# Optimization experiments

Hardware: AMD Instinct MI355X
Metric: run time of the kernel (lower is better)

Reference implementation:

```python
import jax, jax.numpy as jnp
import numpy as np


def setup_inputs() -> dict:
    key = jax.random.key(0)
    k1, k2 = jax.random.split(key)
    B, N = 16, 131072
    x = jax.random.normal(k1, (B, N, 3), dtype=jnp.float32)
    farthest_init = jax.random.randint(k2, (B,), 0, N)  # torch.randint(0, N, (B,))
    return {"x": x, "farthest_init": farthest_init, "npoint": 4096}


def reference(x, farthest_init, npoint):
    """Farthest point sampling: returns sampled point indices [B, npoint].

    npoint corresponds to keypoint_num = int(max(density * volume)) in the
    original module; it is shape-determining so it is passed as a static int.
    """
    xyz = x[:, :, :3]                      # [B, N, 3]
    B, N, _ = xyz.shape
    INF = jnp.float32(1e10)                # matches torch's 1e10 init distance

    def step(carry, _):
        distance, farthest = carry         # [B, N], [B]
        # gather current centroid per batch: xyz[b, farthest[b], :]
        centroid = jnp.take_along_axis(xyz, farthest[:, None, None], axis=1)  # [B,1,3]
        dist = jnp.sum((xyz - centroid) ** 2, axis=-1)  # [B, N]
        distance = jnp.minimum(distance, dist)          # masked update dist<distance
        new_farthest = jnp.argmax(distance, axis=-1)    # [B]
        return (distance, new_farthest), farthest       # emit index chosen this step

    init = (jnp.full((B, N), INF, dtype=xyz.dtype), farthest_init)
    _, centroids = jax.lax.scan(step, init, None, length=npoint)  # [npoint, B]
    return centroids.T                                            # [B, npoint]
```

## Files before the change

kernel.cpp:

```cpp
#include <hip/hip_runtime.h>
#include <stdint.h>

#define NBATCH 16
#define NPTS   131072
#define NPOINT 4096
#define KWG    16
#define TPB    512
#define NWAVE  (TPB/64)
#define PPT    (NPTS/(KWG*TPB))
#define SEG    (NPTS/KWG)
#define SEGSH  13

typedef unsigned long long u64;
typedef unsigned int u32;

template<int CTRL>
__device__ __forceinline__ u32 dpp32(u32 x) {
    return (u32)__builtin_amdgcn_update_dpp(0, (int)x, CTRL, 0xf, 0xf, true);
}
__device__ __forceinline__ u32 umax_(u32 a, u32 b) { return a > b ? a : b; }

template<int CTRL>
__device__ __forceinline__ u64 dpp64max(u64 x) {
    u32 lo = dpp32<CTRL>((u32)x);
    u32 hi = dpp32<CTRL>((u32)(x >> 32));
    u64 o = ((u64)hi << 32) | lo;
    return o > x ? o : x;
}
__device__ __forceinline__ u32 wave_umax(u32 x) {
    x = umax_(x, dpp32<0xB1>(x));
    x = umax_(x, dpp32<0x4E>(x));
    x = umax_(x, dpp32<0x124>(x));
    x = umax_(x, dpp32<0x128>(x));
    x = umax_(x, (u32)__builtin_amdgcn_ds_swizzle((int)x, 0x401F));
    x = umax_(x, (u32)__shfl_xor((int)x, 32, 64));
    return x;
}
__device__ __forceinline__ u64 row16_umax64(u64 k) {
    k = dpp64max<0xB1>(k);
    k = dpp64max<0x4E>(k);
    k = dpp64max<0x124>(k);
    k = dpp64max<0x128>(k);
    return k;
}

__global__ __launch_bounds__(TPB, 2) void fps_kernel(
    const float* __restrict__ xyz, const int* __restrict__ finit,
    int* __restrict__ out, u64* __restrict__ ring)
{
    const int b    = blockIdx.x >> 4;
    const int w    = blockIdx.x & 15;
    const int tid  = threadIdx.x;
    const int lane = tid & 63;
    const int wv   = tid >> 6;

    const float* xb = xyz + (size_t)b * NPTS * 3;
    const int base = w * SEG;

    float px[PPT], py[PPT], pz[PPT], pd[PPT];
    u32 inv[PPT];
    #pragma unroll
    for (int j = 0; j < PPT; ++j) {
        int idx = base + j * TPB + tid;
        px[j] = xb[(size_t)idx * 3 + 0];
        py[j] = xb[(size_t)idx * 3 + 1];
        pz[j] = xb[(size_t)idx * 3 + 2];
        pd[j] = 1e10f;
        inv[j] = (u32)(NPTS - 1 - idx);
    }

    __shared__ u64   lds_keys[NWAVE];
    __shared__ float bc[3];

    const int f0 = finit[b];
    if (w == 0 && tid == 0) out[b * NPOINT] = f0;
    float cx = xb[(size_t)f0 * 3 + 0];
    float cy = xb[(size_t)f0 * 3 + 1];
    float cz = xb[(size_t)f0 * 3 + 2];

    u64* bp = ring + (size_t)b * 2 * KWG;

    for (int t = 1; t < NPOINT; ++t) {
        float m0 = -1.0f, m1 = -1.0f, m2 = -1.0f, m3 = -1.0f;
        #pragma unroll
        for (int j = 0; j < PPT; ++j) {
            float dx = __fsub_rn(px[j], cx);
            float dy = __fsub_rn(py[j], cy);
            float dz = __fsub_rn(pz[j], cz);
            float d  = __fmaf_rn(dz, dz, __fmaf_rn(dy, dy, __fmul_rn(dx, dx)));
            float nd = fminf(pd[j], d);
            pd[j] = nd;
            if ((j & 3) == 0)      m0 = fmaxf(m0, nd);
            else if ((j & 3) == 1) m1 = fmaxf(m1, nd);
            else if ((j & 3) == 2) m2 = fmaxf(m2, nd);
            else                   m3 = fmaxf(m3, nd);
        }
        float mx = fmaxf(fmaxf(m0, m1), fmaxf(m2, m3));
        u32 mxb = wave_umax(__float_as_uint(mx));
        u32 b0 = 0, b1 = 0, b2 = 0, b3 = 0;
        #pragma unroll
        for (int j = 0; j < PPT; ++j) {
            bool tie = (__float_as_uint(pd[j]) == mxb);
            if ((j & 3) == 0)      b0 = tie ? umax_(b0, inv[j]) : b0;
            else if ((j & 3) == 1) b1 = tie ? umax_(b1, inv[j]) : b1;
            else if ((j & 3) == 2) b2 = tie ? umax_(b2, inv[j]) : b2;
            else                   b3 = tie ? umax_(b3, inv[j]) : b3;
        }
        u32 bv = wave_umax(umax_(umax_(b0, b1), umax_(b2, b3)));
        if (lane == 0)
            lds_keys[wv] = ((u64)mxb << 17) | (u64)bv;
        __syncthreads();

        const int p = t & 1;
        if (wv == 0) {
            const u64 tt = (u64)(u32)t;
            const u64 tg = tt << 49;
            u64 kb = lds_keys[lane & (NWAVE - 1)];
            kb = row16_umax64(kb);
            u64* bpp = bp + (p << 4);
            if (lane == 0)
                __hip_atomic_store(&bpp[w], tg | kb, __ATOMIC_RELAXED,
                                   __HIP_MEMORY_SCOPE_AGENT);
            u64 g = tg | kb;
            if (lane < 16 && lane != w) {
                u64* sp = &bpp[lane];
                u64 ga = __hip_atomic_load(sp, __ATOMIC_RELAXED, __HIP_MEMORY_SCOPE_AGENT);
                for (;;) {
                    u64 gb = __hip_atomic_load(sp, __ATOMIC_RELAXED, __HIP_MEMORY_SCOPE_AGENT);
                    if ((ga >> 49) == tt) { g = ga; break; }
                    ga = __hip_atomic_load(sp, __ATOMIC_RELAXED, __HIP_MEMORY_SCOPE_AGENT);
                    if ((gb >> 49) == tt) { g = gb; break; }
                }
            }
            float sxl = 0.f, syl = 0.f, szl = 0.f;
            if (lane < 16) {
                int bi_l = (NPTS - 1) - (int)(g & 0x1FFFF);
                sxl = xb[(size_t)bi_l * 3 + 0];
                syl = xb[(size_t)bi_l * 3 + 1];
                szl = xb[(size_t)bi_l * 3 + 2];
            }
            u64 K = row16_umax64((lane < 16) ? g : 0);
            if (lane < 16) {
                int bi    = (NPTS - 1) - (int)(K & 0x1FFFF);
                int Pstar = bi >> SEGSH;
                float cxn = __shfl(sxl, Pstar, 64);
                float cyn = __shfl(syl, Pstar, 64);
                float czn = __shfl(szl, Pstar, 64);
                if (lane == 0) {
                    bc[0] = cxn; bc[1] = cyn; bc[2] = czn;
                    if (w == 0) out[b * NPOINT + t] = bi;
                }
            }
        }
        __syncthreads();
        cx = bc[0]; cy = bc[1]; cz = bc[2];
    }
}

extern "C" void kernel_launch(void* const* d_in, const int* in_sizes, int n_in,
                              void* d_out, int out_size, void* d_ws, size_t ws_size,
                              hipStream_t stream) {
    const float* xyz   = (const float*)d_in[0];
    const int*   finit = (const int*)d_in[1];
    int*         out   = (int*)d_out;
    u64*         ring  = (u64*)d_ws;

    void* args[] = { (void*)&xyz, (void*)&finit, (void*)&out, (void*)&ring };
    dim3 grid(NBATCH * KWG), block(TPB);
    if (hipLaunchCooperativeKernel((const void*)fps_kernel, grid, block, args, 0, stream)
        != hipSuccess) {
        fps_kernel<<<grid, block, 0, stream>>>(xyz, finit, out, ring);
    }
}
```

Measured before the change: 7.814 ms.

## Publish per-wave argmax keys globally and drop intra-block barrier before exchange

Each wave now writes its own tagged max key straight into a per-batch global ring of 128 slots, instead of first combining keys in LDS behind a __syncthreads. Wave 0 of every workgroup polls all 128 slots, two per lane, and prefetches the candidate centroid coordinates as soon as both of its slots arrive. It then finishes the reduction with a full-wave 64-bit max and picks the winning lane by segment and wave index. The centroid broadcast buffer is double-buffered by parity so that one barrier per step is enough. The aim is to cut one block barrier and the LDS round trip per step, at the cost of eight times more global polling traffic and a larger workspace ring.

```diff
diff --git a/kernel.cpp b/kernel.cpp
--- a/kernel.cpp
+++ b/kernel.cpp
@@ -20,13 +20,6 @@
 }
 __device__ __forceinline__ u32 umax_(u32 a, u32 b) { return a > b ? a : b; }
 
-template<int CTRL>
-__device__ __forceinline__ u64 dpp64max(u64 x) {
-    u32 lo = dpp32<CTRL>((u32)x);
-    u32 hi = dpp32<CTRL>((u32)(x >> 32));
-    u64 o = ((u64)hi << 32) | lo;
-    return o > x ? o : x;
-}
 __device__ __forceinline__ u32 wave_umax(u32 x) {
     x = umax_(x, dpp32<0xB1>(x));
     x = umax_(x, dpp32<0x4E>(x));
@@ -36,11 +29,32 @@
     x = umax_(x, (u32)__shfl_xor((int)x, 32, 64));
     return x;
 }
-__device__ __forceinline__ u64 row16_umax64(u64 k) {
+template<int CTRL>
+__device__ __forceinline__ u64 dpp64max(u64 x) {
+    u32 lo = dpp32<CTRL>((u32)x);
+    u32 hi = dpp32<CTRL>((u32)(x >> 32));
+    u64 o = ((u64)hi << 32) | lo;
+    return o > x ? o : x;
+}
+__device__ __forceinline__ u64 swz64max(u64 x) {
+    u32 lo = (u32)__builtin_amdgcn_ds_swizzle((int)(u32)x, 0x401F);
+    u32 hi = (u32)__builtin_amdgcn_ds_swizzle((int)(u32)(x >> 32), 0x401F);
+    u64 o = ((u64)hi << 32) | lo;
+    return o > x ? o : x;
+}
+__device__ __forceinline__ u64 sx32max(u64 x) {
+    u32 lo = (u32)__shfl_xor((int)(u32)x, 32, 64);
+    u32 hi = (u32)__shfl_xor((int)(u32)(x >> 32), 32, 64);
+    u64 o = ((u64)hi << 32) | lo;
+    return o > x ? o : x;
+}
+__device__ __forceinline__ u64 wave_umax64(u64 k) {
     k = dpp64max<0xB1>(k);
     k = dpp64max<0x4E>(k);
     k = dpp64max<0x124>(k);
     k = dpp64max<0x128>(k);
+    k = swz64max(k);
+    k = sx32max(k);
     return k;
 }
 
@@ -69,8 +83,7 @@
         inv[j] = (u32)(NPTS - 1 - idx);
     }
 
-    __shared__ u64   lds_keys[NWAVE];
-    __shared__ float bc[3];
+    __shared__ float bc[2][3];
 
     const int f0 = finit[b];
     if (w == 0 && tid == 0) out[b * NPOINT] = f0;
@@ -78,7 +91,7 @@
     float cy = xb[(size_t)f0 * 3 + 1];
     float cz = xb[(size_t)f0 * 3 + 2];
 
-    u64* bp = ring + (size_t)b * 2 * KWG;
+    u64* bring = ring + (size_t)b * 2 * 128;
 
     for (int t = 1; t < NPOINT; ++t) {
         float m0 = -1.0f, m1 = -1.0f, m2 = -1.0f, m3 = -1.0f;
@@ -107,53 +120,52 @@
             else                   b3 = tie ? umax_(b3, inv[j]) : b3;
         }
         u32 bv = wave_umax(umax_(umax_(b0, b1), umax_(b2, b3)));
+
+        const int p  = t & 1;
+        const u64 tt = (u64)(u32)t;
+        const u64 tg = tt << 49;
+        u64* bpp = bring + (p << 7);
         if (lane == 0)
-            lds_keys[wv] = ((u64)mxb << 17) | (u64)bv;
-        __syncthreads();
+            __hip_atomic_store(&bpp[(w << 3) | wv],
+                               tg | ((u64)mxb << 17) | (u64)bv,
+                               __ATOMIC_RELAXED, __HIP_MEMORY_SCOPE_AGENT);
 
-        const int p = t & 1;
         if (wv == 0) {
-            const u64 tt = (u64)(u32)t;
-            const u64 tg = tt << 49;
-            u64 kb = lds_keys[lane & (NWAVE - 1)];
-            kb = row16_umax64(kb);
-            u64* bpp = bp + (p << 4);
-            if (lane == 0)
-                __hip_atomic_store(&bpp[w], tg | kb, __ATOMIC_RELAXED,
-                                   __HIP_MEMORY_SCOPE_AGENT);
-            u64 g = tg | kb;
-            if (lane < 16 && lane != w) {
-                u64* sp = &bpp[lane];
-                u64 ga = __hip_atomic_load(sp, __ATOMIC_RELAXED, __HIP_MEMORY_SCOPE_AGENT);
-                for (;;) {
-                    u64 gb = __hip_atomic_load(sp, __ATOMIC_RELAXED, __HIP_MEMORY_SCOPE_AGENT);
-                    if ((ga >> 49) == tt) { g = ga; break; }
-                    ga = __hip_atomic_load(sp, __ATOMIC_RELAXED, __HIP_MEMORY_SCOPE_AGENT);
-                    if ((gb >> 49) == tt) { g = gb; break; }
+            u64* sp0 = bpp + lane;
+            u64* sp1 = bpp + 64 + lane;
+            u64 ga = 0, gb = 0;
+            bool da = false, db = false, pf = false;
+            float sxl = 0.f, syl = 0.f, szl = 0.f;
+            for (;;) {
+                u64 va = da ? ga : __hip_atomic_load(sp0, __ATOMIC_RELAXED, __HIP_MEMORY_SCOPE_AGENT);
+                u64 vb = db ? gb : __hip_atomic_load(sp1, __ATOMIC_RELAXED, __HIP_MEMORY_SCOPE_AGENT);
+                if (!da && (va >> 49) == tt) { ga = va; da = true; }
+                if (!db && (vb >> 49) == tt) { gb = vb; db = true; }
+                if (da && db && !pf) {
+                    pf = true;
+                    u64 gm = ga > gb ? ga : gb;
+                    int bl = (NPTS - 1) - (int)(gm & 0x1FFFF);
+                    const float* cp = &xb[(size_t)bl * 3];
+                    sxl = cp[0]; syl = cp[1]; szl = cp[2];
+                    asm volatile("" : "+v"(sxl), "+v"(syl), "+v"(szl));
                 }
+                if (__all(da && db)) break;
             }
-            float sxl = 0.f, syl = 0.f, szl = 0.f;
-            if (lane < 16) {
-                int bi_l = (NPTS - 1) - (int)(g & 0x1FFFF);
-                sxl = xb[(size_t)bi_l * 3 + 0];
-                syl = xb[(size_t)bi_l * 3 + 1];
-                szl = xb[(size_t)bi_l * 3 + 2];
-            }
-            u64 K = row16_umax64((lane < 16) ? g : 0);
-            if (lane < 16) {
-                int bi    = (NPTS - 1) - (int)(K & 0x1FFFF);
-                int Pstar = bi >> SEGSH;
-                float cxn = __shfl(sxl, Pstar, 64);
-                float cyn = __shfl(syl, Pstar, 64);
-                float czn = __shfl(szl, Pstar, 64);
-                if (lane == 0) {
-                    bc[0] = cxn; bc[1] = cyn; bc[2] = czn;
-                    if (w == 0) out[b * NPOINT + t] = bi;
-                }
+            u64 g = ga > gb ? ga : gb;
+            u64 K  = wave_umax64(g);
+            int bi = (NPTS - 1) - (int)(K & 0x1FFFF);
+            int s     = ((bi >> SEGSH) << 3) | ((bi >> 6) & (NWAVE - 1));
+            int lstar = s & 63;
+            float cxn = __shfl(sxl, lstar, 64);
+            float cyn = __shfl(syl, lstar, 64);
+            float czn = __shfl(szl, lstar, 64);
+            if (lane == 0) {
+                bc[p][0] = cxn; bc[p][1] = cyn; bc[p][2] = czn;
+                if (w == 0) out[b * NPOINT + t] = bi;
             }
         }
         __syncthreads();
-        cx = bc[0]; cy = bc[1]; cz = bc[2];
+        cx = bc[p][0]; cy = bc[p][1]; cz = bc[p][2];
     }
 }
 
```

New measurement: 11.78 ms. 50.8% more time.

## Replace block barriers with tagged LDS flags and pass winner coordinates in keys

Applied to the files above, without the earlier changes.

Each wave now picks the coordinates of its own argmax candidate from registers and shuffles them out. It publishes the key and the coordinates as tagged 64-bit words in LDS. Wave 0 polls these words instead of waiting at `__syncthreads`, then exchanges key and coordinates with the peer workgroups through the global ring. This removes the dependent global gather of the winning point's xyz on every iteration. The other waves spin on a release/acquire-tagged broadcast slot instead of a second barrier, which takes both block-wide barriers off the serial critical path. The cost is more cross-workgroup ring traffic (four words per workgroup) and extra selection and shuffle work per step.

```diff
diff --git a/kernel.cpp b/kernel.cpp
--- a/kernel.cpp
+++ b/kernel.cpp
@@ -14,19 +14,18 @@
 typedef unsigned long long u64;
 typedef unsigned int u32;
 
+#define LDA(p)    __hip_atomic_load((p),  __ATOMIC_RELAXED, __HIP_MEMORY_SCOPE_AGENT)
+#define STA(p,v)  __hip_atomic_store((p),(v),__ATOMIC_RELAXED,__HIP_MEMORY_SCOPE_AGENT)
+#define LDW(p)    __hip_atomic_load((p),  __ATOMIC_RELAXED, __HIP_MEMORY_SCOPE_WORKGROUP)
+#define LDWA(p)   __hip_atomic_load((p),  __ATOMIC_ACQUIRE, __HIP_MEMORY_SCOPE_WORKGROUP)
+#define STW(p,v)  __hip_atomic_store((p),(v),__ATOMIC_RELAXED,__HIP_MEMORY_SCOPE_WORKGROUP)
+#define STWR(p,v) __hip_atomic_store((p),(v),__ATOMIC_RELEASE,__HIP_MEMORY_SCOPE_WORKGROUP)
+
 template<int CTRL>
 __device__ __forceinline__ u32 dpp32(u32 x) {
     return (u32)__builtin_amdgcn_update_dpp(0, (int)x, CTRL, 0xf, 0xf, true);
 }
 __device__ __forceinline__ u32 umax_(u32 a, u32 b) { return a > b ? a : b; }
-
-template<int CTRL>
-__device__ __forceinline__ u64 dpp64max(u64 x) {
-    u32 lo = dpp32<CTRL>((u32)x);
-    u32 hi = dpp32<CTRL>((u32)(x >> 32));
-    u64 o = ((u64)hi << 32) | lo;
-    return o > x ? o : x;
-}
 __device__ __forceinline__ u32 wave_umax(u32 x) {
     x = umax_(x, dpp32<0xB1>(x));
     x = umax_(x, dpp32<0x4E>(x));
@@ -36,6 +35,13 @@
     x = umax_(x, (u32)__shfl_xor((int)x, 32, 64));
     return x;
 }
+template<int CTRL>
+__device__ __forceinline__ u64 dpp64max(u64 x) {
+    u32 lo = dpp32<CTRL>((u32)x);
+    u32 hi = dpp32<CTRL>((u32)(x >> 32));
+    u64 o = ((u64)hi << 32) | lo;
+    return o > x ? o : x;
+}
 __device__ __forceinline__ u64 row16_umax64(u64 k) {
     k = dpp64max<0xB1>(k);
     k = dpp64max<0x4E>(k);
@@ -43,6 +49,21 @@
     k = dpp64max<0x128>(k);
     return k;
 }
+__device__ __forceinline__ u64 shfl_u64(u64 v, int s) {
+    u32 lo = (u32)__shfl((int)(u32)v, s, 64);
+    u32 hi = (u32)__shfl((int)(u32)(v >> 32), s, 64);
+    return ((u64)hi << 32) | lo;
+}
+
+#define SEL16(arr,k,out_) do { \
+    float a0=((k)&1)?arr[1]:arr[0];  float a1=((k)&1)?arr[3]:arr[2];   \
+    float a2=((k)&1)?arr[5]:arr[4];  float a3=((k)&1)?arr[7]:arr[6];   \
+    float a4=((k)&1)?arr[9]:arr[8];  float a5=((k)&1)?arr[11]:arr[10]; \
+    float a6=((k)&1)?arr[13]:arr[12];float a7=((k)&1)?arr[15]:arr[14]; \
+    float b0_=((k)&2)?a1:a0; float b1_=((k)&2)?a3:a2; \
+    float b2_=((k)&2)?a5:a4; float b3_=((k)&2)?a7:a6; \
+    float c0_=((k)&4)?b1_:b0_; float c1_=((k)&4)?b3_:b2_; \
+    out_=((k)&8)?c1_:c0_; } while(0)
 
 __global__ __launch_bounds__(TPB, 2) void fps_kernel(
     const float* __restrict__ xyz, const int* __restrict__ finit,
@@ -69,8 +90,8 @@
         inv[j] = (u32)(NPTS - 1 - idx);
     }
 
-    __shared__ u64   lds_keys[NWAVE];
-    __shared__ float bc[3];
+    __shared__ u64 s1[NWAVE * 4];
+    __shared__ u64 sbc[3];
 
     const int f0 = finit[b];
     if (w == 0 && tid == 0) out[b * NPOINT] = f0;
@@ -78,7 +99,7 @@
     float cy = xb[(size_t)f0 * 3 + 1];
     float cz = xb[(size_t)f0 * 3 + 2];
 
-    u64* bp = ring + (size_t)b * 2 * KWG;
+    u64* bring = ring + (size_t)b * 2 * KWG * 4;
 
     for (int t = 1; t < NPOINT; ++t) {
         float m0 = -1.0f, m1 = -1.0f, m2 = -1.0f, m3 = -1.0f;
@@ -107,53 +128,77 @@
             else                   b3 = tie ? umax_(b3, inv[j]) : b3;
         }
         u32 bv = wave_umax(umax_(umax_(b0, b1), umax_(b2, b3)));
-        if (lane == 0)
-            lds_keys[wv] = ((u64)mxb << 17) | (u64)bv;
-        __syncthreads();
-
-        const int p = t & 1;
+
+        const u64 tt  = (u64)(u32)t;
+        const u64 tg  = tt << 49;
+        int local    = ((NPTS - 1) - (int)bv) - base;
+        int jwin     = local >> 9;
+        int lane_win = local & 63;
+        float sx, sy, sz;
+        SEL16(px, jwin, sx); SEL16(py, jwin, sy); SEL16(pz, jwin, sz);
+        sx = __shfl(sx, lane_win, 64);
+        sy = __shfl(sy, lane_win, 64);
+        sz = __shfl(sz, lane_win, 64);
+        u64 sval = (lane == 0) ? (tg | ((u64)mxb << 17) | (u64)bv)
+                 : (lane == 1) ? (tg | ((u64)__float_as_uint(sx) << 17))
+                 : (lane == 2) ? (tg | ((u64)__float_as_uint(sy) << 17))
+                 :               (tg | ((u64)__float_as_uint(sz) << 17));
+        if (lane < 4) STW(&s1[(wv << 2) | lane], sval);
+
         if (wv == 0) {
-            const u64 tt = (u64)(u32)t;
-            const u64 tg = tt << 49;
-            u64 kb = lds_keys[lane & (NWAVE - 1)];
-            kb = row16_umax64(kb);
-            u64* bpp = bp + (p << 4);
-            if (lane == 0)
-                __hip_atomic_store(&bpp[w], tg | kb, __ATOMIC_RELAXED,
-                                   __HIP_MEMORY_SCOPE_AGENT);
-            u64 g = tg | kb;
-            if (lane < 16 && lane != w) {
-                u64* sp = &bpp[lane];
-                u64 ga = __hip_atomic_load(sp, __ATOMIC_RELAXED, __HIP_MEMORY_SCOPE_AGENT);
+            u64 g1 = 0;
+            if (lane < 32) {
+                u64* a = &s1[((lane & 7) << 2) | (lane >> 3)];
+                do { g1 = LDW(a); } while ((g1 >> 49) != tt);
+            }
+            u64 kred = (lane < 8) ? g1 : 0;
+            kred = row16_umax64(kred);
+            u64 kb = shfl_u64(kred, 0);
+            int bidx = (NPTS - 1) - (int)(kb & 0x1FFFF);
+            int Wst  = ((bidx - base) >> 6) & (NWAVE - 1);
+            u64 vX = shfl_u64(g1, 8 + Wst);
+            u64 vY = shfl_u64(g1, 16 + Wst);
+            u64 vZ = shfl_u64(g1, 24 + Wst);
+            u64* bpp = bring + ((size_t)(t & 1) << 6);
+            u64 pval = (lane == 0) ? kb : (lane == 1) ? vX : (lane == 2) ? vY : vZ;
+            if (lane < 4) STA(&bpp[(w << 2) | lane], pval);
+            const int peer = lane & 15, word = lane >> 4;
+            u64 g = (word == 0) ? kb : (word == 1) ? vX : (word == 2) ? vY : vZ;
+            if (peer != w) {
+                u64* sp = &bpp[(peer << 2) | word];
+                u64 ga = LDA(sp);
                 for (;;) {
-                    u64 gb = __hip_atomic_load(sp, __ATOMIC_RELAXED, __HIP_MEMORY_SCOPE_AGENT);
+                    u64 gb = LDA(sp);
                     if ((ga >> 49) == tt) { g = ga; break; }
-                    ga = __hip_atomic_load(sp, __ATOMIC_RELAXED, __HIP_MEMORY_SCOPE_AGENT);
+                    ga = LDA(sp);
                     if ((gb >> 49) == tt) { g = gb; break; }
                 }
             }
-            float sxl = 0.f, syl = 0.f, szl = 0.f;
-            if (lane < 16) {
-                int bi_l = (NPTS - 1) - (int)(g & 0x1FFFF);
-                sxl = xb[(size_t)bi_l * 3 + 0];
-                syl = xb[(size_t)bi_l * 3 + 1];
-                szl = xb[(size_t)bi_l * 3 + 2];
+            u64 K2 = row16_umax64((lane < 16) ? g : 0);
+            u64 K0 = shfl_u64(K2, 0);
+            int bi   = (NPTS - 1) - (int)(K0 & 0x1FFFF);
+            int Pst  = bi >> SEGSH;
+            u64 gx = shfl_u64(g, 16 + Pst);
+            u64 gy = shfl_u64(g, 32 + Pst);
+            u64 gz = shfl_u64(g, 48 + Pst);
+            if (lane == 0) {
+                STW(&sbc[0], gx);
+                STW(&sbc[1], gy);
+                STWR(&sbc[2], gz);
+                if (w == 0) out[b * NPOINT + t] = bi;
             }
-            u64 K = row16_umax64((lane < 16) ? g : 0);
-            if (lane < 16) {
-                int bi    = (NPTS - 1) - (int)(K & 0x1FFFF);
-                int Pstar = bi >> SEGSH;
-                float cxn = __shfl(sxl, Pstar, 64);
-                float cyn = __shfl(syl, Pstar, 64);
-                float czn = __shfl(szl, Pstar, 64);
-                if (lane == 0) {
-                    bc[0] = cxn; bc[1] = cyn; bc[2] = czn;
-                    if (w == 0) out[b * NPOINT + t] = bi;
-                }
-            }
+            cx = __uint_as_float((u32)(gx >> 17));
+            cy = __uint_as_float((u32)(gy >> 17));
+            cz = __uint_as_float((u32)(gz >> 17));
+        } else {
+            u64 gz;
+            do { gz = LDWA(&sbc[2]); } while ((gz >> 49) != tt);
+            u64 gx = LDW(&sbc[0]);
+            u64 gy = LDW(&sbc[1]);
+            cx = __uint_as_float((u32)(gx >> 17));
+            cy = __uint_as_float((u32)(gy >> 17));
+            cz = __uint_as_float((u32)(gz >> 17));
         }
-        __syncthreads();
-        cx = bc[0]; cy = bc[1]; cz = bc[2];
     }
 }
 
```

Result: slower. 10.44 ms (+33.6%).

## Publish winner coordinates through the exchange ring to avoid post-sync global gather

Applied to the files above, without the earlier changes.

Each wave now pulls its local winner's xyz out of registers with a select tree and a cross-lane shuffle, and stashes them in LDS. Each workgroup then publishes its best key plus the three coordinates as tagged 64-bit words in a larger ring. After the inter-workgroup spin exchange, the chosen centroid is taken from the polled values by shuffle. This removes the dependent global load of candidate coordinates that sat on the serial critical path of every FPS step. In exchange there are four times as many polled ring slots, extra select and shuffle work per step, and a larger workspace footprint.

```diff
diff --git a/kernel.cpp b/kernel.cpp
--- a/kernel.cpp
+++ b/kernel.cpp
@@ -20,13 +20,6 @@
 }
 __device__ __forceinline__ u32 umax_(u32 a, u32 b) { return a > b ? a : b; }
 
-template<int CTRL>
-__device__ __forceinline__ u64 dpp64max(u64 x) {
-    u32 lo = dpp32<CTRL>((u32)x);
-    u32 hi = dpp32<CTRL>((u32)(x >> 32));
-    u64 o = ((u64)hi << 32) | lo;
-    return o > x ? o : x;
-}
 __device__ __forceinline__ u32 wave_umax(u32 x) {
     x = umax_(x, dpp32<0xB1>(x));
     x = umax_(x, dpp32<0x4E>(x));
@@ -36,6 +29,13 @@
     x = umax_(x, (u32)__shfl_xor((int)x, 32, 64));
     return x;
 }
+template<int CTRL>
+__device__ __forceinline__ u64 dpp64max(u64 x) {
+    u32 lo = dpp32<CTRL>((u32)x);
+    u32 hi = dpp32<CTRL>((u32)(x >> 32));
+    u64 o = ((u64)hi << 32) | lo;
+    return o > x ? o : x;
+}
 __device__ __forceinline__ u64 row16_umax64(u64 k) {
     k = dpp64max<0xB1>(k);
     k = dpp64max<0x4E>(k);
@@ -43,6 +43,21 @@
     k = dpp64max<0x128>(k);
     return k;
 }
+__device__ __forceinline__ u64 shfl_u64(u64 v, int s) {
+    u32 lo = (u32)__shfl((int)(u32)v, s, 64);
+    u32 hi = (u32)__shfl((int)(u32)(v >> 32), s, 64);
+    return ((u64)hi << 32) | lo;
+}
+
+#define SEL16(arr,k,out_) do { \
+    float a0=((k)&1)?arr[1]:arr[0];  float a1=((k)&1)?arr[3]:arr[2];   \
+    float a2=((k)&1)?arr[5]:arr[4];  float a3=((k)&1)?arr[7]:arr[6];   \
+    float a4=((k)&1)?arr[9]:arr[8];  float a5=((k)&1)?arr[11]:arr[10]; \
+    float a6=((k)&1)?arr[13]:arr[12];float a7=((k)&1)?arr[15]:arr[14]; \
+    float b0_=((k)&2)?a1:a0; float b1_=((k)&2)?a3:a2; \
+    float b2_=((k)&2)?a5:a4; float b3_=((k)&2)?a7:a6; \
+    float c0_=((k)&4)?b1_:b0_; float c1_=((k)&4)?b3_:b2_; \
+    out_=((k)&8)?c1_:c0_; } while(0)
 
 __global__ __launch_bounds__(TPB, 2) void fps_kernel(
     const float* __restrict__ xyz, const int* __restrict__ finit,
@@ -70,6 +85,7 @@
     }
 
     __shared__ u64   lds_keys[NWAVE];
+    __shared__ float lds_cx[NWAVE], lds_cy[NWAVE], lds_cz[NWAVE];
     __shared__ float bc[3];
 
     const int f0 = finit[b];
@@ -78,7 +94,7 @@
     float cy = xb[(size_t)f0 * 3 + 1];
     float cz = xb[(size_t)f0 * 3 + 2];
 
-    u64* bp = ring + (size_t)b * 2 * KWG;
+    u64* bp = ring + (size_t)b * 2 * 64;
 
     for (int t = 1; t < NPOINT; ++t) {
         float m0 = -1.0f, m1 = -1.0f, m2 = -1.0f, m3 = -1.0f;
@@ -107,8 +123,18 @@
             else                   b3 = tie ? umax_(b3, inv[j]) : b3;
         }
         u32 bv = wave_umax(umax_(umax_(b0, b1), umax_(b2, b3)));
-        if (lane == 0)
+        int local    = ((NPTS - 1) - (int)bv) - base;
+        int jwin     = local >> 9;
+        int lane_win = local & 63;
+        float sx, sy, sz;
+        SEL16(px, jwin, sx); SEL16(py, jwin, sy); SEL16(pz, jwin, sz);
+        sx = __shfl(sx, lane_win, 64);
+        sy = __shfl(sy, lane_win, 64);
+        sz = __shfl(sz, lane_win, 64);
+        if (lane == 0) {
             lds_keys[wv] = ((u64)mxb << 17) | (u64)bv;
+            lds_cx[wv] = sx; lds_cy[wv] = sy; lds_cz[wv] = sz;
+        }
         __syncthreads();
 
         const int p = t & 1;
@@ -117,13 +143,24 @@
             const u64 tg = tt << 49;
             u64 kb = lds_keys[lane & (NWAVE - 1)];
             kb = row16_umax64(kb);
-            u64* bpp = bp + (p << 4);
-            if (lane == 0)
-                __hip_atomic_store(&bpp[w], tg | kb, __ATOMIC_RELAXED,
-                                   __HIP_MEMORY_SCOPE_AGENT);
-            u64 g = tg | kb;
-            if (lane < 16 && lane != w) {
-                u64* sp = &bpp[lane];
+            int blocal = ((NPTS - 1) - (int)(kb & 0x1FFFF)) - base;
+            int Wst    = (blocal >> 6) & (NWAVE - 1);
+            float wx = lds_cx[Wst], wy = lds_cy[Wst], wz = lds_cz[Wst];
+            u64* bpp = bp + (p << 6);
+            u64 pval = (lane == 0) ? (tg | kb)
+                     : (lane == 1) ? (tg | ((u64)__float_as_uint(wx) << 17))
+                     : (lane == 2) ? (tg | ((u64)__float_as_uint(wy) << 17))
+                     :               (tg | ((u64)__float_as_uint(wz) << 17));
+            if (lane < 4)
+                __hip_atomic_store(&bpp[(lane << 4) | w], pval,
+                                   __ATOMIC_RELAXED, __HIP_MEMORY_SCOPE_AGENT);
+            const int peer = lane & 15, word = lane >> 4;
+            u64 g = (word == 0) ? (tg | kb)
+                  : (word == 1) ? (tg | ((u64)__float_as_uint(wx) << 17))
+                  : (word == 2) ? (tg | ((u64)__float_as_uint(wy) << 17))
+                  :               (tg | ((u64)__float_as_uint(wz) << 17));
+            if (peer != w) {
+                u64* sp = &bpp[(word << 4) | peer];
                 u64 ga = __hip_atomic_load(sp, __ATOMIC_RELAXED, __HIP_MEMORY_SCOPE_AGENT);
                 for (;;) {
                     u64 gb = __hip_atomic_load(sp, __ATOMIC_RELAXED, __HIP_MEMORY_SCOPE_AGENT);
@@ -132,24 +169,18 @@
                     if ((gb >> 49) == tt) { g = gb; break; }
                 }
             }
-            float sxl = 0.f, syl = 0.f, szl = 0.f;
-            if (lane < 16) {
-                int bi_l = (NPTS - 1) - (int)(g & 0x1FFFF);
-                sxl = xb[(size_t)bi_l * 3 + 0];
-                syl = xb[(size_t)bi_l * 3 + 1];
-                szl = xb[(size_t)bi_l * 3 + 2];
-            }
-            u64 K = row16_umax64((lane < 16) ? g : 0);
-            if (lane < 16) {
-                int bi    = (NPTS - 1) - (int)(K & 0x1FFFF);
-                int Pstar = bi >> SEGSH;
-                float cxn = __shfl(sxl, Pstar, 64);
-                float cyn = __shfl(syl, Pstar, 64);
-                float czn = __shfl(szl, Pstar, 64);
-                if (lane == 0) {
-                    bc[0] = cxn; bc[1] = cyn; bc[2] = czn;
-                    if (w == 0) out[b * NPOINT + t] = bi;
-                }
+            u64 K  = row16_umax64((lane < 16) ? g : 0);
+            u64 K0 = shfl_u64(K, 0);
+            int bi    = (NPTS - 1) - (int)(K0 & 0x1FFFF);
+            int Pstar = bi >> SEGSH;
+            u64 gx = shfl_u64(g, 16 + Pstar);
+            u64 gy = shfl_u64(g, 32 + Pstar);
+            u64 gz = shfl_u64(g, 48 + Pstar);
+            if (lane == 0) {
+                bc[0] = __uint_as_float((u32)(gx >> 17));
+                bc[1] = __uint_as_float((u32)(gy >> 17));
+                bc[2] = __uint_as_float((u32)(gz >> 17));
+                if (w == 0) out[b * NPOINT + t] = bi;
             }
         }
         __syncthreads();
```

After: 9.574 ms. 22.5% more time.
